# Kernel tuning notes

Measured on AMD Instinct MI355X. Metric: run time of the kernel, lower is better.

Reference implementation:

```python
import jax, jax.numpy as jnp
import numpy as np
import math

ANCHORS = np.array([[12., 16.], [19., 36.], [40., 28.]], dtype=np.float32)
NUM_CLASSES = 80
IMG_DIM = 608.0
NUM_ANCHORS = 3


def setup_inputs() -> dict:
    key = jax.random.key(0)
    ks = jax.random.split(key, 9)
    B, A, G, NC = 16, NUM_ANCHORS, 76, NUM_CLASSES
    x = jax.random.normal(ks[0], (B, A * (NC + 5), G, G), jnp.float32)
    iou = jax.random.uniform(ks[1], (B, A, G, G), jnp.float32, 0.0, 0.95)
    obj_mask = jax.random.bernoulli(ks[2], 0.02, (B, A, G, G))
    noobj_mask = jnp.logical_and(~obj_mask, jax.random.bernoulli(ks[3], 0.95, (B, A, G, G)))
    tw = jax.random.uniform(ks[4], (B, A, G, G), jnp.float32, 0.1, 4.0)
    th = jax.random.uniform(ks[5], (B, A, G, G), jnp.float32, 0.1, 4.0)
    tcls = jax.random.uniform(ks[6], (B, A, G, G, NC), jnp.float32)
    tconf = jax.random.uniform(ks[7], (B, A, G, G), jnp.float32)
    tb = jax.random.uniform(ks[8], (B, A, G, G, 4), jnp.float32)
    # target boxes in grid units: centers in [0,G), sizes in (0.5, 8.5)
    target_boxes = jnp.concatenate([tb[..., :2] * G, tb[..., 2:] * 8.0 + 0.5], -1)
    return {"x": x, "iou": iou, "obj_mask": obj_mask, "noobj_mask": noobj_mask,
            "tw": tw, "th": th, "tcls": tcls, "tconf": tconf, "target_boxes": target_boxes}


def _clog(p):
    # torch F.binary_cross_entropy clamps log to -100
    return jnp.maximum(jnp.log(p), -100.0)


def _bce(p, t):
    return -(t * _clog(p) + (1.0 - t) * _clog(1.0 - p))


def yolo_forward(x, iou, obj_mask, noobj_mask, tw, th, tcls, tconf, target_boxes):
    B = x.shape[0]
    G = x.shape[2]
    A, NC = NUM_ANCHORS, NUM_CLASSES
    stride = IMG_DIM / G
    # [B, A, G, G, 5+NC]
    pred = x.reshape(B, A, NC + 5, G, G).transpose(0, 1, 3, 4, 2)
    px = jax.nn.sigmoid(pred[..., 0])
    py = jax.nn.sigmoid(pred[..., 1])
    pw = pred[..., 2]
    ph = pred[..., 3]
    pconf = jax.nn.sigmoid(pred[..., 4])
    pcls = jax.nn.sigmoid(pred[..., 5:])

    scaled = jnp.asarray(ANCHORS) / stride
    gx = jnp.arange(G, dtype=x.dtype)[None, None, None, :]
    gy = jnp.arange(G, dtype=x.dtype)[None, None, :, None]
    aw = scaled[:, 0][None, :, None, None]
    ah = scaled[:, 1][None, :, None, None]

    bx = px + gx
    by = py + gy
    bw = jnp.exp(pw) * aw
    bh = jnp.exp(ph) * ah
    pred_boxes = jnp.stack([bx, by, bw, bh], -1)

    output = jnp.concatenate([
        pred_boxes.reshape(B, -1, 4) * stride,
        pconf.reshape(B, -1, 1),
        pcls.reshape(B, -1, NC)], -1)

    # ---- loss (masked CIoU + BCE), computed dense then mask-reduced ----
    m = obj_mask.astype(x.dtype)
    nm = noobj_mask.astype(x.dtype)
    txc, tyc, twd, tht = (target_boxes[..., i] for i in range(4))

    tx1, ty1 = txc - twd / 2, tyc - tht / 2
    tx2, ty2 = txc + twd / 2, tyc + tht / 2
    px1, py1 = bx - bw / 2, by - bh / 2
    px2, py2 = bx + bw / 2, by + bh / 2

    xc1 = jnp.minimum(px1, tx1)
    yc1 = jnp.minimum(py1, ty1)
    xc2 = jnp.maximum(px2, tx2)
    yc2 = jnp.maximum(py2, ty2)

    c = (xc2 - xc1) ** 2 + (yc2 - yc1) ** 2 + 1e-07
    d = (txc - bx) ** 2 + (tyc - by) ** 2
    rDIoU = d / c
    v = (4.0 / math.pi ** 2) * (jnp.arctan(tw / th) - jnp.arctan(pw / ph)) ** 2
    S = 1.0 - iou
    alpha = jax.lax.stop_gradient(v / (S + v))  # torch.no_grad() block
    ciou_term = 1.0 - iou + rDIoU + alpha * v
    CIoUloss = jnp.sum(m * ciou_term) / B

    cnt_obj = jnp.maximum(jnp.sum(m), 1.0)
    cnt_noobj = jnp.maximum(jnp.sum(nm), 1.0)
    bce_conf = _bce(pconf, tconf)
    loss_conf = 1.0 * jnp.sum(m * bce_conf) / cnt_obj + 100.0 * jnp.sum(nm * bce_conf) / cnt_noobj
    loss_cls = jnp.sum(m[..., None] * _bce(pcls, tcls)) / (cnt_obj * NUM_CLASSES)

    total_loss = CIoUloss + loss_conf + loss_cls
    return output, total_loss


def reference(x, iou, obj_mask, noobj_mask, tw, th, tcls, tconf, target_boxes):
    return yolo_forward(x, iou, obj_mask, noobj_mask, tw, th, tcls, tconf, target_boxes)
```

## Files before the change

### kernel.cpp

```cpp
#include <hip/hip_runtime.h>

#define B_ 16
#define A_ 3
#define G_ 76
#define GG_ (G_*G_)
#define NC_ 80
#define C_ 85
#define NCELL (B_*A_*GG_)
#define OUTN ((size_t)NCELL*C_)
#define NBLKM (NCELL/64)
#define WSLOT 340

typedef float f4 __attribute__((ext_vector_type(4)));

__device__ __forceinline__ float sigf(float v){ return 1.0f/(1.0f + __expf(-v)); }
__device__ __forceinline__ float clog_(float p){ return fmaxf(__logf(p), -100.0f); }
__device__ __forceinline__ float bcef(float p, float t){ return -(t*clog_(p) + (1.0f-t)*clog_(1.0f-p)); }

__global__ __launch_bounds__(256, 7) void mega_kernel(
        const float* __restrict__ x, const float* __restrict__ iou,
        const unsigned int* __restrict__ om, const unsigned int* __restrict__ nm,
        const float* __restrict__ tw, const float* __restrict__ th,
        const float* __restrict__ tcls, const float* __restrict__ tconf,
        const float* __restrict__ tbox,
        float* __restrict__ out, float* __restrict__ partials){
    __shared__ __align__(16) float lds[4][16*C_];
    __shared__ float praw[64][2];
    __shared__ float sred[4][6];

    const int tid  = (int)threadIdx.x;
    const int w    = tid >> 6;
    const int lane = tid & 63;

    unsigned qd8 = NBLKM >> 3, rr = NBLKM & 7u;
    unsigned xcd = blockIdx.x & 7u, seq = blockIdx.x >> 3;
    int blk = (int)((xcd < rr ? xcd*(qd8+1u) : rr*(qd8+1u) + (xcd-rr)*qd8) + seq);

    int nw  = blk*64 + w*16;
    int ba  = nw / GG_;
    int ijw = nw - ba*GG_;
    int a   = ba % A_;
    float aw8 = (a==0)?12.0f:((a==1)?19.0f:40.0f);
    float ah8 = (a==0)?16.0f:((a==1)?36.0f:28.0f);
    const float* xw = x + (size_t)ba*C_*GG_ + (size_t)ijw;
    float* ldsw = lds[w];

    f4 rv[6];
    #pragma unroll
    for (int it=0; it<6; ++it){
        int s = lane + it*64;
        if (s < WSLOT){
            int k = s >> 2, q = s & 3;
            rv[it] = *(const f4*)(xw + (size_t)k*GG_ + 4*q);
        }
    }

    #pragma unroll
    for (int it=0; it<6; ++it){
        int s = lane + it*64;
        if (s < WSLOT){
            int k = s >> 2, q = s & 3;
            int ij0 = ijw + 4*q;
            f4 v = rv[it];
            f4 r;
            if (k >= 4){
                r[0]=sigf(v[0]); r[1]=sigf(v[1]); r[2]=sigf(v[2]); r[3]=sigf(v[3]);
            } else if (k == 0){
                float j0 = (float)(ij0 - (ij0/G_)*G_);
                r[0]=(sigf(v[0])+j0)*8.0f;      r[1]=(sigf(v[1])+j0+1.0f)*8.0f;
                r[2]=(sigf(v[2])+j0+2.0f)*8.0f; r[3]=(sigf(v[3])+j0+3.0f)*8.0f;
            } else if (k == 1){
                float fi = (float)(ij0/G_);
                r[0]=(sigf(v[0])+fi)*8.0f; r[1]=(sigf(v[1])+fi)*8.0f;
                r[2]=(sigf(v[2])+fi)*8.0f; r[3]=(sigf(v[3])+fi)*8.0f;
            } else if (k == 2){
                r[0]=__expf(v[0])*aw8; r[1]=__expf(v[1])*aw8;
                r[2]=__expf(v[2])*aw8; r[3]=__expf(v[3])*aw8;
                int c0 = w*16 + 4*q;
                praw[c0+0][0]=v[0]; praw[c0+1][0]=v[1];
                praw[c0+2][0]=v[2]; praw[c0+3][0]=v[3];
            } else {
                r[0]=__expf(v[0])*ah8; r[1]=__expf(v[1])*ah8;
                r[2]=__expf(v[2])*ah8; r[3]=__expf(v[3])*ah8;
                int c0 = w*16 + 4*q;
                praw[c0+0][1]=v[0]; praw[c0+1][1]=v[1];
                praw[c0+2][1]=v[2]; praw[c0+3][1]=v[3];
            }
            int bix = 4*q*C_ + k;
            ldsw[bix]      = r[0];
            ldsw[bix+C_]   = r[1];
            ldsw[bix+2*C_] = r[2];
            ldsw[bix+3*C_] = r[3];
        }
    }

    {
        const f4* src4 = (const f4*)ldsw;
        f4* dst4 = (f4*)(out + (size_t)nw*C_);
        #pragma unroll
        for (int it=0; it<6; ++it){
            int s = lane + it*64;
            if (s < WSLOT) dst4[s] = src4[s];
        }
    }

    int lc = lane >> 2, qd = lane & 3;
    int n  = nw + lc;
    bool obj   = om[n] != 0u;
    bool noobj = nm[n] != 0u;
    const float* lrow = ldsw + lc*C_;

    float cls = 0.f;
    if (obj){
        const float* tcl = tcls + (size_t)n*NC_ + qd*20;
        const float* lp  = lrow + 5 + qd*20;
        #pragma unroll 4
        for (int j=0; j<20; ++j) cls += bcef(lp[j], tcl[j]);
    }
    cls += __shfl_xor(cls, 1, 64);
    cls += __shfl_xor(cls, 2, 64);
    if (qd != 0) cls = 0.f;

    float ciou=0.f, co=0.f, cn=0.f;
    if (qd == 0 && obj){
        float bx = lrow[0]*0.125f, by = lrow[1]*0.125f;
        float bw = lrow[2]*0.125f, bh = lrow[3]*0.125f;
        float rwv = praw[w*16+lc][0], rhv = praw[w*16+lc][1];
        float iouv = iou[n], twv = tw[n], thv = th[n];
        f4 tb = *(const f4*)(tbox + (size_t)n*4);
        float txc=tb[0], tyc=tb[1], twd=tb[2], tht=tb[3];
        float tx1 = txc - twd*0.5f, ty1 = tyc - tht*0.5f;
        float tx2 = txc + twd*0.5f, ty2 = tyc + tht*0.5f;
        float px1 = bx - bw*0.5f,  py1 = by - bh*0.5f;
        float px2 = bx + bw*0.5f,  py2 = by + bh*0.5f;
        float xc1 = fminf(px1, tx1), yc1 = fminf(py1, ty1);
        float xc2 = fmaxf(px2, tx2), yc2 = fmaxf(py2, ty2);
        float cc = (xc2-xc1)*(xc2-xc1) + (yc2-yc1)*(yc2-yc1) + 1e-7f;
        float dd = (txc-bx)*(txc-bx) + (tyc-by)*(tyc-by);
        float rdiou = dd/cc;
        float dat = atanf(twv/thv) - atanf(rwv/rhv);
        float vv = 0.40528473456935108577f * dat*dat;
        float Si = 1.0f - iouv;
        float alpha = vv/(Si+vv);
        ciou = 1.0f - iouv + rdiou + alpha*vv;
    }
    if (qd == 1 && (obj || noobj)){
        float bc = bcef(lrow[4], tconf[n]);
        co = obj ? bc : 0.f;
        cn = noobj ? bc : 0.f;
    }
    unsigned long long bo  = __ballot(obj   && qd == 0);
    unsigned long long bn2 = __ballot(noobj && qd == 1);

    float vals[4] = {ciou, co, cn, cls};
    #pragma unroll
    for (int q2=0; q2<4; ++q2){
        float v = vals[q2];
        #pragma unroll
        for (int o=32; o>0; o>>=1) v += __shfl_xor(v, o, 64);
        vals[q2] = v;
    }
    if (lane == 0){
        sred[w][0]=vals[0]; sred[w][1]=vals[1]; sred[w][2]=vals[2]; sred[w][3]=vals[3];
        sred[w][4]=(float)__popcll(bo); sred[w][5]=(float)__popcll(bn2);
    }
    __syncthreads();
    if (tid < 6)
        partials[(size_t)tid*NBLKM + blk] = sred[0][tid]+sred[1][tid]+sred[2][tid]+sred[3][tid];
}

__global__ __launch_bounds__(256) void final_kernel(const float* __restrict__ partials,
                                                    float* __restrict__ out_loss){
    double acc[6] = {0,0,0,0,0,0};
    for (int idx = (int)threadIdx.x; idx < NBLKM; idx += 256){
        #pragma unroll
        for (int q=0;q<6;q++) acc[q] += (double)partials[(size_t)q*NBLKM + idx];
    }
    #pragma unroll
    for (int q=0;q<6;q++){
        double v = acc[q];
        #pragma unroll
        for (int o=32;o>0;o>>=1) v += __shfl_xor(v, o, 64);
        acc[q] = v;
    }
    __shared__ double smd[6][4];
    int lane = (int)threadIdx.x & 63, wid = (int)threadIdx.x >> 6;
    if (lane == 0){
        #pragma unroll
        for (int q=0;q<6;q++) smd[q][wid] = acc[q];
    }
    __syncthreads();
    if (threadIdx.x == 0){
        double s[6];
        #pragma unroll
        for (int q=0;q<6;q++) s[q] = smd[q][0]+smd[q][1]+smd[q][2]+smd[q][3];
        double cnt_o = fmax(s[4], 1.0);
        double cnt_n = fmax(s[5], 1.0);
        double total = s[0]/(double)B_
                     + s[1]/cnt_o
                     + 100.0*s[2]/cnt_n
                     + s[3]/(cnt_o*(double)NC_);
        *out_loss = (float)total;
    }
}

extern "C" void kernel_launch(void* const* d_in, const int* in_sizes, int n_in,
                              void* d_out, int out_size, void* d_ws, size_t ws_size,
                              hipStream_t stream){
    const float* x     = (const float*)d_in[0];
    const float* iou   = (const float*)d_in[1];
    const unsigned int* om = (const unsigned int*)d_in[2];
    const unsigned int* nm = (const unsigned int*)d_in[3];
    const float* tw    = (const float*)d_in[4];
    const float* th    = (const float*)d_in[5];
    const float* tcls  = (const float*)d_in[6];
    const float* tconf = (const float*)d_in[7];
    const float* tbox  = (const float*)d_in[8];
    float* out = (float*)d_out;

    float* partials = (float*)d_ws;

    mega_kernel<<<NBLKM, 256, 0, stream>>>(x, iou, om, nm, tw, th, tcls, tconf, tbox,
                                           out, partials);
    final_kernel<<<1, 256, 0, stream>>>(partials, out + OUTN);
}
```

Measured before the change: 50.46 us.

## Process two 16-cell tiles per wave, prefetching both before compute

Each wave now handles 32 cells as two 16-cell tiles. Loads for both tiles, plus the mask and tconf values, are issued before any compute so more memory traffic is in flight per wave, and the block count is halved. The LDS staging buffer is reused across the two tiles in turn, and the loss partial sums accumulate across both tiles. In exchange the kernel holds twice the prefetch registers and occupancy is lowered to 4 blocks per SIMD, which may reduce latency hiding across waves.

```diff
diff --git a/kernel.cpp b/kernel.cpp
--- a/kernel.cpp
+++ b/kernel.cpp
@@ -8,7 +8,7 @@
 #define C_ 85
 #define NCELL (B_*A_*GG_)
 #define OUTN ((size_t)NCELL*C_)
-#define NBLKM (NCELL/64)
+#define NBLK (NCELL/128)
 #define WSLOT 340
 
 typedef float f4 __attribute__((ext_vector_type(4)));
@@ -17,7 +17,7 @@
 __device__ __forceinline__ float clog_(float p){ return fmaxf(__logf(p), -100.0f); }
 __device__ __forceinline__ float bcef(float p, float t){ return -(t*clog_(p) + (1.0f-t)*clog_(1.0f-p)); }
 
-__global__ __launch_bounds__(256, 7) void mega_kernel(
+__global__ __launch_bounds__(256, 4) void mega_kernel(
         const float* __restrict__ x, const float* __restrict__ iou,
         const unsigned int* __restrict__ om, const unsigned int* __restrict__ nm,
         const float* __restrict__ tw, const float* __restrict__ th,
@@ -25,134 +25,150 @@
         const float* __restrict__ tbox,
         float* __restrict__ out, float* __restrict__ partials){
     __shared__ __align__(16) float lds[4][16*C_];
-    __shared__ float praw[64][2];
+    __shared__ float praw[4][16][2];
     __shared__ float sred[4][6];
 
     const int tid  = (int)threadIdx.x;
     const int w    = tid >> 6;
     const int lane = tid & 63;
 
-    unsigned qd8 = NBLKM >> 3, rr = NBLKM & 7u;
+    unsigned qq = NBLK >> 3, rr = NBLK & 7u;
     unsigned xcd = blockIdx.x & 7u, seq = blockIdx.x >> 3;
-    int blk = (int)((xcd < rr ? xcd*(qd8+1u) : rr*(qd8+1u) + (xcd-rr)*qd8) + seq);
-
-    int nw  = blk*64 + w*16;
-    int ba  = nw / GG_;
-    int ijw = nw - ba*GG_;
-    int a   = ba % A_;
-    float aw8 = (a==0)?12.0f:((a==1)?19.0f:40.0f);
-    float ah8 = (a==0)?16.0f:((a==1)?36.0f:28.0f);
-    const float* xw = x + (size_t)ba*C_*GG_ + (size_t)ijw;
+    int blk = (int)((xcd < rr ? xcd*(qq+1u) : rr*(qq+1u) + (xcd-rr)*qq) + seq);
+
+    int nwave = blk*128 + w*32;
     float* ldsw = lds[w];
 
-    f4 rv[6];
-    #pragma unroll
-    for (int it=0; it<6; ++it){
-        int s = lane + it*64;
-        if (s < WSLOT){
-            int k = s >> 2, q = s & 3;
-            rv[it] = *(const f4*)(xw + (size_t)k*GG_ + 4*q);
-        }
-    }
-
-    #pragma unroll
-    for (int it=0; it<6; ++it){
-        int s = lane + it*64;
-        if (s < WSLOT){
-            int k = s >> 2, q = s & 3;
-            int ij0 = ijw + 4*q;
-            f4 v = rv[it];
-            f4 r;
-            if (k >= 4){
-                r[0]=sigf(v[0]); r[1]=sigf(v[1]); r[2]=sigf(v[2]); r[3]=sigf(v[3]);
-            } else if (k == 0){
-                float j0 = (float)(ij0 - (ij0/G_)*G_);
-                r[0]=(sigf(v[0])+j0)*8.0f;      r[1]=(sigf(v[1])+j0+1.0f)*8.0f;
-                r[2]=(sigf(v[2])+j0+2.0f)*8.0f; r[3]=(sigf(v[3])+j0+3.0f)*8.0f;
-            } else if (k == 1){
-                float fi = (float)(ij0/G_);
-                r[0]=(sigf(v[0])+fi)*8.0f; r[1]=(sigf(v[1])+fi)*8.0f;
-                r[2]=(sigf(v[2])+fi)*8.0f; r[3]=(sigf(v[3])+fi)*8.0f;
-            } else if (k == 2){
-                r[0]=__expf(v[0])*aw8; r[1]=__expf(v[1])*aw8;
-                r[2]=__expf(v[2])*aw8; r[3]=__expf(v[3])*aw8;
-                int c0 = w*16 + 4*q;
-                praw[c0+0][0]=v[0]; praw[c0+1][0]=v[1];
-                praw[c0+2][0]=v[2]; praw[c0+3][0]=v[3];
-            } else {
-                r[0]=__expf(v[0])*ah8; r[1]=__expf(v[1])*ah8;
-                r[2]=__expf(v[2])*ah8; r[3]=__expf(v[3])*ah8;
-                int c0 = w*16 + 4*q;
-                praw[c0+0][1]=v[0]; praw[c0+1][1]=v[1];
-                praw[c0+2][1]=v[2]; praw[c0+3][1]=v[3];
-            }
-            int bix = 4*q*C_ + k;
-            ldsw[bix]      = r[0];
-            ldsw[bix+C_]   = r[1];
-            ldsw[bix+2*C_] = r[2];
-            ldsw[bix+3*C_] = r[3];
-        }
-    }
-
-    {
-        const f4* src4 = (const f4*)ldsw;
-        f4* dst4 = (f4*)(out + (size_t)nw*C_);
+    f4 rv[2][6];
+    #pragma unroll
+    for (int t=0; t<2; ++t){
+        int nt = nwave + t*16;
+        int ba = nt / GG_;
+        int ij = nt - ba*GG_;
+        const float* xw = x + (size_t)ba*C_*GG_ + (size_t)ij;
         #pragma unroll
         for (int it=0; it<6; ++it){
             int s = lane + it*64;
-            if (s < WSLOT) dst4[s] = src4[s];
-        }
-    }
-
-    int lc = lane >> 2, qd = lane & 3;
-    int n  = nw + lc;
-    bool obj   = om[n] != 0u;
-    bool noobj = nm[n] != 0u;
-    const float* lrow = ldsw + lc*C_;
-
-    float cls = 0.f;
-    if (obj){
-        const float* tcl = tcls + (size_t)n*NC_ + qd*20;
-        const float* lp  = lrow + 5 + qd*20;
-        #pragma unroll 4
-        for (int j=0; j<20; ++j) cls += bcef(lp[j], tcl[j]);
-    }
-    cls += __shfl_xor(cls, 1, 64);
-    cls += __shfl_xor(cls, 2, 64);
-    if (qd != 0) cls = 0.f;
-
-    float ciou=0.f, co=0.f, cn=0.f;
-    if (qd == 0 && obj){
-        float bx = lrow[0]*0.125f, by = lrow[1]*0.125f;
-        float bw = lrow[2]*0.125f, bh = lrow[3]*0.125f;
-        float rwv = praw[w*16+lc][0], rhv = praw[w*16+lc][1];
-        float iouv = iou[n], twv = tw[n], thv = th[n];
-        f4 tb = *(const f4*)(tbox + (size_t)n*4);
-        float txc=tb[0], tyc=tb[1], twd=tb[2], tht=tb[3];
-        float tx1 = txc - twd*0.5f, ty1 = tyc - tht*0.5f;
-        float tx2 = txc + twd*0.5f, ty2 = tyc + tht*0.5f;
-        float px1 = bx - bw*0.5f,  py1 = by - bh*0.5f;
-        float px2 = bx + bw*0.5f,  py2 = by + bh*0.5f;
-        float xc1 = fminf(px1, tx1), yc1 = fminf(py1, ty1);
-        float xc2 = fmaxf(px2, tx2), yc2 = fmaxf(py2, ty2);
-        float cc = (xc2-xc1)*(xc2-xc1) + (yc2-yc1)*(yc2-yc1) + 1e-7f;
-        float dd = (txc-bx)*(txc-bx) + (tyc-by)*(tyc-by);
-        float rdiou = dd/cc;
-        float dat = atanf(twv/thv) - atanf(rwv/rhv);
-        float vv = 0.40528473456935108577f * dat*dat;
-        float Si = 1.0f - iouv;
-        float alpha = vv/(Si+vv);
-        ciou = 1.0f - iouv + rdiou + alpha*vv;
-    }
-    if (qd == 1 && (obj || noobj)){
-        float bc = bcef(lrow[4], tconf[n]);
-        co = obj ? bc : 0.f;
-        cn = noobj ? bc : 0.f;
-    }
-    unsigned long long bo  = __ballot(obj   && qd == 0);
-    unsigned long long bn2 = __ballot(noobj && qd == 1);
-
-    float vals[4] = {ciou, co, cn, cls};
+            if (s < WSLOT){
+                int k = s >> 2, q = s & 3;
+                rv[t][it] = *(const f4*)(xw + (size_t)k*GG_ + 4*q);
+            }
+        }
+    }
+    const int lc = lane >> 2, qd = lane & 3;
+    bool objt[2], nobt[2];
+    float tcf[2];
+    #pragma unroll
+    for (int t=0; t<2; ++t){
+        int n = nwave + t*16 + lc;
+        objt[t] = om[n] != 0u;
+        nobt[t] = nm[n] != 0u;
+        tcf[t]  = tconf[n];
+    }
+
+    float accC=0.f, accO=0.f, accN=0.f, accL=0.f, cntO=0.f, cntN=0.f;
+
+    #pragma unroll
+    for (int t=0; t<2; ++t){
+        int nt  = nwave + t*16;
+        int ba  = nt / GG_;
+        int ijw = nt - ba*GG_;
+        int a   = ba % A_;
+        float aw8 = (a==0)?12.0f:((a==1)?19.0f:40.0f);
+        float ah8 = (a==0)?16.0f:((a==1)?36.0f:28.0f);
+
+        #pragma unroll
+        for (int it=0; it<6; ++it){
+            int s = lane + it*64;
+            if (s < WSLOT){
+                int k = s >> 2, q = s & 3;
+                int ij0 = ijw + 4*q;
+                f4 v = rv[t][it];
+                f4 r;
+                if (k >= 4){
+                    r[0]=sigf(v[0]); r[1]=sigf(v[1]); r[2]=sigf(v[2]); r[3]=sigf(v[3]);
+                } else if (k == 0){
+                    float j0 = (float)(ij0 - (ij0/G_)*G_);
+                    r[0]=(sigf(v[0])+j0)*8.0f;      r[1]=(sigf(v[1])+j0+1.0f)*8.0f;
+                    r[2]=(sigf(v[2])+j0+2.0f)*8.0f; r[3]=(sigf(v[3])+j0+3.0f)*8.0f;
+                } else if (k == 1){
+                    float fi = (float)(ij0/G_);
+                    r[0]=(sigf(v[0])+fi)*8.0f; r[1]=(sigf(v[1])+fi)*8.0f;
+                    r[2]=(sigf(v[2])+fi)*8.0f; r[3]=(sigf(v[3])+fi)*8.0f;
+                } else if (k == 2){
+                    r[0]=__expf(v[0])*aw8; r[1]=__expf(v[1])*aw8;
+                    r[2]=__expf(v[2])*aw8; r[3]=__expf(v[3])*aw8;
+                    int c0 = 4*q;
+                    praw[w][c0+0][0]=v[0]; praw[w][c0+1][0]=v[1];
+                    praw[w][c0+2][0]=v[2]; praw[w][c0+3][0]=v[3];
+                } else {
+                    r[0]=__expf(v[0])*ah8; r[1]=__expf(v[1])*ah8;
+                    r[2]=__expf(v[2])*ah8; r[3]=__expf(v[3])*ah8;
+                    int c0 = 4*q;
+                    praw[w][c0+0][1]=v[0]; praw[w][c0+1][1]=v[1];
+                    praw[w][c0+2][1]=v[2]; praw[w][c0+3][1]=v[3];
+                }
+                int bix = 4*q*C_ + k;
+                ldsw[bix]      = r[0];
+                ldsw[bix+C_]   = r[1];
+                ldsw[bix+2*C_] = r[2];
+                ldsw[bix+3*C_] = r[3];
+            }
+        }
+
+        {
+            const f4* src4 = (const f4*)ldsw;
+            f4* dst4 = (f4*)(out + (size_t)nt*C_);
+            #pragma unroll
+            for (int it=0; it<6; ++it){
+                int s = lane + it*64;
+                if (s < WSLOT) dst4[s] = src4[s];
+            }
+        }
+
+        bool obj = objt[t], noobj = nobt[t];
+        int n = nt + lc;
+        const float* lrow = ldsw + lc*C_;
+        if (obj){
+            const float* tcl = tcls + (size_t)n*NC_ + qd*20;
+            const float* lp  = lrow + 5 + qd*20;
+            float cls = 0.f;
+            #pragma unroll 4
+            for (int j=0; j<20; ++j) cls += bcef(lp[j], tcl[j]);
+            accL += cls;
+        }
+        if (qd == 0 && obj){
+            float bx = lrow[0]*0.125f, by = lrow[1]*0.125f;
+            float bw = lrow[2]*0.125f, bh = lrow[3]*0.125f;
+            float rwv = praw[w][lc][0], rhv = praw[w][lc][1];
+            float iouv = iou[n], twv = tw[n], thv = th[n];
+            f4 tb = *(const f4*)(tbox + (size_t)n*4);
+            float txc=tb[0], tyc=tb[1], twd=tb[2], tht=tb[3];
+            float tx1 = txc - twd*0.5f, ty1 = tyc - tht*0.5f;
+            float tx2 = txc + twd*0.5f, ty2 = tyc + tht*0.5f;
+            float px1 = bx - bw*0.5f,  py1 = by - bh*0.5f;
+            float px2 = bx + bw*0.5f,  py2 = by + bh*0.5f;
+            float xc1 = fminf(px1, tx1), yc1 = fminf(py1, ty1);
+            float xc2 = fmaxf(px2, tx2), yc2 = fmaxf(py2, ty2);
+            float cc = (xc2-xc1)*(xc2-xc1) + (yc2-yc1)*(yc2-yc1) + 1e-7f;
+            float dd = (txc-bx)*(txc-bx) + (tyc-by)*(tyc-by);
+            float rdiou = dd/cc;
+            float dat = atanf(twv/thv) - atanf(rwv/rhv);
+            float vv = 0.40528473456935108577f * dat*dat;
+            float Si = 1.0f - iouv;
+            float alpha = vv/(Si+vv);
+            accC += 1.0f - iouv + rdiou + alpha*vv;
+        }
+        if (qd == 1 && (obj || noobj)){
+            float bc = bcef(lrow[4], tcf[t]);
+            if (obj)   accO += bc;
+            if (noobj) accN += bc;
+        }
+        cntO += (float)__popcll(__ballot(obj   && qd == 0));
+        cntN += (float)__popcll(__ballot(noobj && qd == 1));
+    }
+
+    float vals[4] = {accC, accO, accN, accL};
     #pragma unroll
     for (int q2=0; q2<4; ++q2){
         float v = vals[q2];
@@ -162,19 +178,19 @@
     }
     if (lane == 0){
         sred[w][0]=vals[0]; sred[w][1]=vals[1]; sred[w][2]=vals[2]; sred[w][3]=vals[3];
-        sred[w][4]=(float)__popcll(bo); sred[w][5]=(float)__popcll(bn2);
+        sred[w][4]=cntO;    sred[w][5]=cntN;
     }
     __syncthreads();
     if (tid < 6)
-        partials[(size_t)tid*NBLKM + blk] = sred[0][tid]+sred[1][tid]+sred[2][tid]+sred[3][tid];
+        partials[(size_t)tid*NBLK + blk] = sred[0][tid]+sred[1][tid]+sred[2][tid]+sred[3][tid];
 }
 
 __global__ __launch_bounds__(256) void final_kernel(const float* __restrict__ partials,
                                                     float* __restrict__ out_loss){
     double acc[6] = {0,0,0,0,0,0};
-    for (int idx = (int)threadIdx.x; idx < NBLKM; idx += 256){
-        #pragma unroll
-        for (int q=0;q<6;q++) acc[q] += (double)partials[(size_t)q*NBLKM + idx];
+    for (int idx = (int)threadIdx.x; idx < NBLK; idx += 256){
+        #pragma unroll
+        for (int q=0;q<6;q++) acc[q] += (double)partials[(size_t)q*NBLK + idx];
     }
     #pragma unroll
     for (int q=0;q<6;q++){
@@ -220,7 +236,7 @@
 
     float* partials = (float*)d_ws;
 
-    mega_kernel<<<NBLKM, 256, 0, stream>>>(x, iou, om, nm, tw, th, tcls, tconf, tbox,
-                                           out, partials);
+    mega_kernel<<<NBLK, 256, 0, stream>>>(x, iou, om, nm, tw, th, tcls, tconf, tbox,
+                                          out, partials);
     final_kernel<<<1, 256, 0, stream>>>(partials, out + OUTN);
 }
```

Result: slower. 54.61 us (+8.2%).
